# Optimization experiments

Hardware: AMD Instinct MI355X
Metric: run time of the kernel (lower is better)

Reference implementation:

```python
import jax, jax.numpy as jnp
import numpy as np

DIM = 1024
DIM_HEAD = 64
HEADS = 16
BATCH = 2
SEQ = 2048
SCALE = DIM_HEAD ** -0.5


def setup_inputs() -> dict:
    key = jax.random.key(0)
    ks = jax.random.split(key, 5)
    tokens = jax.random.normal(ks[0], (BATCH, SEQ, DIM), dtype=jnp.float32)
    wq = jax.random.normal(ks[1], (HEADS, DIM, DIM_HEAD), dtype=jnp.float32)
    wk = jax.random.normal(ks[2], (HEADS, DIM, DIM_HEAD), dtype=jnp.float32)
    wv = jax.random.normal(ks[3], (HEADS, DIM, DIM_HEAD), dtype=jnp.float32)
    wo = jax.random.normal(ks[4], (HEADS, DIM_HEAD, DIM), dtype=jnp.float32)
    return {"tokens": tokens, "wq": wq, "wk": wk, "wv": wv, "wo": wo}


def reference(tokens, wq, wk, wv, wo):
    # q, k, v: [b, h, n, dh]
    q = jnp.einsum('bnd,hde->bhne', tokens, wq) * SCALE
    k = jnp.einsum('bnd,hde->bhne', tokens, wk)
    v = jnp.einsum('bnd,hde->bhne', tokens, wv)
    sim = jnp.einsum('bhie,bhje->bhij', q, k)          # [b, h, n, n]
    attn = jax.nn.softmax(sim, axis=-1)
    aggregated = jnp.einsum('bhij,bhje->bhie', attn, v)  # [b, h, n, dh]
    retrieved = jnp.einsum('bhne,hed->bnd', aggregated, wo)  # sum over heads
    return retrieved
```

## Files before the change

kernel.cpp:

```cpp
#include <hip/hip_runtime.h>
#include <hip/hip_fp16.h>
#include <stdint.h>

#define BB 2
#define HH 16
#define SS 2048
#define DD 1024
#define DHH 64
#define QSCALE 0.18033688011112042f

typedef _Float16 half8 __attribute__((ext_vector_type(8)));
typedef _Float16 half4 __attribute__((ext_vector_type(4)));
typedef __fp16 fp16x2 __attribute__((ext_vector_type(2)));
typedef float floatx4 __attribute__((ext_vector_type(4)));

__device__ __forceinline__ floatx4 mfma16(half8 a, half8 b, floatx4 c) {
  return __builtin_amdgcn_mfma_f32_16x16x32_f16(a, b, c, 0, 0, 0);
}
__device__ __forceinline__ floatx4 mfma16k16(half4 a, half4 b, floatx4 c) {
  return __builtin_amdgcn_mfma_f32_16x16x16f16(a, b, c, 0, 0, 0);
}

__device__ __forceinline__ void dma16(const _Float16* g, _Float16* l) {
  __builtin_amdgcn_global_load_lds(
      (const __attribute__((address_space(1))) uint32_t*)g,
      (__attribute__((address_space(3))) uint32_t*)l,
      16, 0, 0);
}

__global__ __launch_bounds__(256) void convert_kernel(
    const float* __restrict__ wq, const float* __restrict__ wk,
    const float* __restrict__ wv, const float* __restrict__ wo,
    _Float16* __restrict__ Wh, _Float16* __restrict__ Wl,
    _Float16* __restrict__ Wot)
{
  __shared__ float St[64][68];
  const int kt = blockIdx.x;
  const int hy = blockIdx.y;
  const int z  = blockIdx.z;
  const int t  = (int)threadIdx.x;
  const int k0 = kt * 64;

  const float* src = (z == 0) ? (wq + hy * (DD * DHH))
                   : (z == 1) ? (wk + hy * (DD * DHH))
                   : (z == 2) ? (wv + hy * (DD * DHH))
                   : wo;

  const int rr = t >> 4, cc = (t & 15) * 4;
  if (z < 3) {
    #pragma unroll
    for (int i = 0; i < 4; ++i)
      *(floatx4*)&St[rr + 16 * i][cc] =
          *(const floatx4*)(src + (k0 + rr + 16 * i) * DHH + cc);
  } else {
    const int d0 = hy * 64;
    #pragma unroll
    for (int i = 0; i < 4; ++i)
      *(floatx4*)&St[rr + 16 * i][cc] =
          *(const floatx4*)(src + (k0 + rr + 16 * i) * 1024 + d0 + cc);
  }
  __syncthreads();

  const int e = t >> 2, kc = (t & 3) * 16;
  if (z < 3) {
    const int n = z * 1024 + hy * 64 + e;
    half8 hi0, hi1, lo0, lo1;
    #pragma unroll
    for (int u = 0; u < 16; ++u) {
      float x = St[kc + u][e];
      _Float16 hh = (_Float16)x;
      _Float16 ll = (_Float16)(x - (float)hh);
      if (u < 8) { hi0[u] = hh; lo0[u] = ll; }
      else       { hi1[u - 8] = hh; lo1[u - 8] = ll; }
    }
    *(half8*)(Wh + n * 1024 + k0 + kc)     = hi0;
    *(half8*)(Wh + n * 1024 + k0 + kc + 8) = hi1;
    *(half8*)(Wl + n * 1024 + k0 + kc)     = lo0;
    *(half8*)(Wl + n * 1024 + k0 + kc + 8) = lo1;
  } else {
    const int d0 = hy * 64;
    half8 hi0, hi1;
    #pragma unroll
    for (int u = 0; u < 16; ++u) {
      _Float16 hh = (_Float16)St[kc + u][e];
      if (u < 8) hi0[u] = hh; else hi1[u - 8] = hh;
    }
    *(half8*)(Wot + (d0 + e) * 1024 + k0 + kc)     = hi0;
    *(half8*)(Wot + (d0 + e) * 1024 + k0 + kc + 8) = hi1;
  }
}

__global__ __launch_bounds__(256) void tokens_split_kernel(
    const float* __restrict__ tokens,
    _Float16* __restrict__ th, _Float16* __restrict__ tl)
{
  const int i = ((int)blockIdx.x * 256 + (int)threadIdx.x) * 8;
  floatx4 x0 = *(const floatx4*)(tokens + i);
  floatx4 x1 = *(const floatx4*)(tokens + i + 4);
  half8 h, l;
  #pragma unroll
  for (int j = 0; j < 8; ++j) {
    float x = (j < 4) ? x0[j] : x1[j - 4];
    _Float16 hh = (_Float16)x;
    h[j] = hh;
    l[j] = (_Float16)(x - (float)hh);
  }
  *(half8*)(th + i) = h;
  *(half8*)(tl + i) = l;
}

__global__ __launch_bounds__(256) void qkv_gemm_kernel(
    const _Float16* __restrict__ th, const _Float16* __restrict__ tl,
    const _Float16* __restrict__ Wh, const _Float16* __restrict__ Wl,
    _Float16* __restrict__ qh, _Float16* __restrict__ ql,
    _Float16* __restrict__ kh, _Float16* __restrict__ kl,
    _Float16* __restrict__ vt)
{
  __shared__ alignas(16) _Float16 sbuf[2][4][128 * 32];

  const int n0 = blockIdx.x * 128;
  const int m0 = blockIdx.y * 128;
  const int zb = n0 >> 10;
  const bool is_v = (zb == 2);
  const int t = (int)threadIdx.x;
  const int lane = t & 63, wid = t >> 6;
  const int l16 = lane & 15, q4 = lane >> 4;
  const int mw = (wid & 1) * 64, nw = (wid >> 1) * 64;

  const int g  = (lane & 7) ^ ((lane >> 3) & 7);
  const int grow  = (lane >> 3) * 2 + (g >> 2);
  const int gcol8 = (g & 3) * 8;
  const int laneoff = (l16 >> 1) * 128 + (((((l16 & 1) << 2) | q4) ^ (l16 >> 1)) * 16);

  const _Float16* src;
  int arr;
  if (wid == 0)      { src = th + m0 * 1024; arr = 0; }
  else if (wid == 1) { src = Wh + n0 * 1024; arr = 1; }
  else if (wid == 2) { src = Wl + n0 * 1024; arr = 2; }
  else               { src = tl + m0 * 1024; arr = 3; }
  const bool stage_active = !(is_v && wid == 3);
  const _Float16* gsrc = src + grow * 1024 + gcol8;

  const floatx4 z4 = {0.0f, 0.0f, 0.0f, 0.0f};
  floatx4 acc[4][4];
  #pragma unroll
  for (int mi = 0; mi < 4; ++mi)
    #pragma unroll
    for (int ni = 0; ni < 4; ++ni) acc[mi][ni] = z4;

  auto stage = [&](int buf, int kt2) {
    if (stage_active) {
      const _Float16* gp = gsrc + kt2 * 32;
      _Float16* dst = &sbuf[buf][arr][0];
      #pragma unroll
      for (int j = 0; j < 8; ++j)
        dma16(gp + j * 16 * 1024, dst + j * 16 * 32);
    }
  };

  auto compute = [&](int buf) {
    const char* sAh = (const char*)&sbuf[buf][0][0];
    const char* sBh = (const char*)&sbuf[buf][1][0];
    const char* sBl = (const char*)&sbuf[buf][2][0];
    const char* sAl = (const char*)&sbuf[buf][3][0];
    half8 a_h[4];
    #pragma unroll
    for (int mi = 0; mi < 4; ++mi)
      a_h[mi] = *(const half8*)(sAh + (mw + mi * 16) * 64 + laneoff);
    if (!is_v) {
      half8 a_l[4];
      #pragma unroll
      for (int mi = 0; mi < 4; ++mi)
        a_l[mi] = *(const half8*)(sAl + (mw + mi * 16) * 64 + laneoff);
      #pragma unroll
      for (int ni = 0; ni < 4; ++ni) {
        const half8 b_h = *(const half8*)(sBh + (nw + ni * 16) * 64 + laneoff);
        const half8 b_l = *(const half8*)(sBl + (nw + ni * 16) * 64 + laneoff);
        #pragma unroll
        for (int mi = 0; mi < 4; ++mi) {
          acc[mi][ni] = mfma16(a_h[mi], b_h, acc[mi][ni]);
          acc[mi][ni] = mfma16(a_h[mi], b_l, acc[mi][ni]);
          acc[mi][ni] = mfma16(a_l[mi], b_h, acc[mi][ni]);
        }
      }
    } else {
      #pragma unroll
      for (int ni = 0; ni < 4; ++ni) {
        const half8 b_h = *(const half8*)(sBh + (nw + ni * 16) * 64 + laneoff);
        const half8 b_l = *(const half8*)(sBl + (nw + ni * 16) * 64 + laneoff);
        #pragma unroll
        for (int mi = 0; mi < 4; ++mi) {
          acc[mi][ni] = mfma16(a_h[mi], b_h, acc[mi][ni]);
          acc[mi][ni] = mfma16(a_h[mi], b_l, acc[mi][ni]);
        }
      }
    }
  };

  stage(0, 0);
  __syncthreads();

  #pragma unroll 1
  for (int kt = 0; kt < 32; kt += 2) {
    if (kt + 1 < 32) stage(1, kt + 1);
    compute(0);
    __syncthreads();
    if (kt + 2 < 32) stage(0, kt + 2);
    compute(1);
    __syncthreads();
  }

  #pragma unroll
  for (int ni = 0; ni < 4; ++ni) {
    const int ncol = n0 + nw + ni * 16;
    const int h = (ncol >> 6) & 15;
    const int e = (ncol & 63) + l16;
    #pragma unroll
    for (int mi = 0; mi < 4; ++mi) {
      #pragma unroll
      for (int r = 0; r < 4; ++r) {
        const int grow2 = m0 + mw + mi * 16 + q4 * 4 + r;
        const int b = grow2 >> 11, s = grow2 & 2047;
        const float v = acc[mi][ni][r];
        const int qkidx = ((b * HH + h) * SS + s) * DHH + e;
        if (zb == 0) {
          const float vs = v * QSCALE;
          const _Float16 hh = (_Float16)vs;
          qh[qkidx] = hh;
          ql[qkidx] = (_Float16)(vs - (float)hh);
        } else if (zb == 1) {
          const _Float16 hh = (_Float16)v;
          kh[qkidx] = hh;
          kl[qkidx] = (_Float16)(v - (float)hh);
        } else {
          vt[((b * HH + h) * DHH + e) * SS + s] = (_Float16)v;
        }
      }
    }
  }
}

__global__ __launch_bounds__(512) void attn_kernel(
    const _Float16* __restrict__ qh, const _Float16* __restrict__ ql,
    const _Float16* __restrict__ kh, const _Float16* __restrict__ kl,
    const _Float16* __restrict__ vt, _Float16* __restrict__ agg)
{
  __shared__ _Float16 Kh[2][64][72], Kl[2][64][72], Vs[2][64][72];

  const int qt = blockIdx.x;
  const int h  = blockIdx.y;
  const int b  = blockIdx.z;
  const int bh = b * HH + h;
  const int t = (int)threadIdx.x;
  const int lane = t & 63, wid = t >> 6;
  const int l16 = lane & 15, q4 = lane >> 4;

  const int sr = t >> 3, sc = (t & 7) * 8;

  half8 qfh[2], qfl[2];
  {
    const int s = qt * 128 + wid * 16 + l16;
    const int base = (bh * SS + s) * DHH + q4 * 8;
    qfh[0] = *(const half8*)(qh + base);
    qfh[1] = *(const half8*)(qh + base + 32);
    qfl[0] = *(const half8*)(ql + base);
    qfl[1] = *(const half8*)(ql + base + 32);
  }

  const floatx4 z4 = {0.0f, 0.0f, 0.0f, 0.0f};
  floatx4 o[4];
  #pragma unroll
  for (int i = 0; i < 4; ++i) o[i] = z4;
  float m_r = -1e30f;
  float l_lane = 0.0f;

  half8 pK, pL, pV;
  {
    const int gk = (bh * SS + sr) * DHH + sc;
    pK = *(const half8*)(kh + gk);
    pL = *(const half8*)(kl + gk);
    pV = *(const half8*)(vt + (bh * DHH + sr) * SS + sc);
  }

  auto body = [&](int buf, int kt) {
    *(half8*)&Kh[buf][sr][sc] = pK;
    *(half8*)&Kl[buf][sr][sc] = pL;
    *(half8*)&Vs[buf][sr][sc] = pV;
    __syncthreads();

    if (kt < 31) {
      const int k1 = (kt + 1) * 64;
      const int gk = (bh * SS + k1 + sr) * DHH + sc;
      pK = *(const half8*)(kh + gk);
      pL = *(const half8*)(kl + gk);
      pV = *(const half8*)(vt + (bh * DHH + sr) * SS + k1 + sc);
    }

    floatx4 sv[4];
    __builtin_amdgcn_s_setprio(1);
    #pragma unroll
    for (int sub = 0; sub < 4; ++sub) {
      const half8 ah0 = *(const half8*)&Kh[buf][sub * 16 + l16][q4 * 8];
      const half8 ah1 = *(const half8*)&Kh[buf][sub * 16 + l16][q4 * 8 + 32];
      const half8 al0 = *(const half8*)&Kl[buf][sub * 16 + l16][q4 * 8];
      const half8 al1 = *(const half8*)&Kl[buf][sub * 16 + l16][q4 * 8 + 32];
      floatx4 s4 = z4;
      s4 = mfma16(ah0, qfh[0], s4);
      s4 = mfma16(ah1, qfh[1], s4);
      s4 = mfma16(al0, qfh[0], s4);
      s4 = mfma16(al1, qfh[1], s4);
      s4 = mfma16(ah0, qfl[0], s4);
      s4 = mfma16(ah1, qfl[1], s4);
      sv[sub] = s4;
    }
    __builtin_amdgcn_s_setprio(0);

    float m0 = fmaxf(fmaxf(sv[0][0], sv[0][1]), fmaxf(sv[0][2], sv[0][3]));
    float m1 = fmaxf(fmaxf(sv[1][0], sv[1][1]), fmaxf(sv[1][2], sv[1][3]));
    float m2 = fmaxf(fmaxf(sv[2][0], sv[2][1]), fmaxf(sv[2][2], sv[2][3]));
    float m3 = fmaxf(fmaxf(sv[3][0], sv[3][1]), fmaxf(sv[3][2], sv[3][3]));
    const float mx = fmaxf(fmaxf(m0, m1), fmaxf(m2, m3));

    if (__any(mx > m_r + 8.0f)) {
      float mc = fmaxf(mx, __shfl_xor(mx, 16));
      mc = fmaxf(mc, __shfl_xor(mc, 32));
      const float mnew = fmaxf(m_r, mc);
      const float alpha = exp2f(m_r - mnew);
      m_r = mnew;
      l_lane *= alpha;
      #pragma unroll
      for (int sub = 0; sub < 4; ++sub)
        #pragma unroll
        for (int r = 0; r < 4; ++r) o[sub][r] *= alpha;
    }

    half4 p4[4];
    #pragma unroll
    for (int c = 0; c < 4; ++c) {
      const float p0 = exp2f(sv[c][0] - m_r);
      const float p1 = exp2f(sv[c][1] - m_r);
      const float p2 = exp2f(sv[c][2] - m_r);
      const float p3 = exp2f(sv[c][3] - m_r);
      l_lane += (p0 + p1) + (p2 + p3);
      const fp16x2 a01 = __builtin_amdgcn_cvt_pkrtz(p0, p1);
      const fp16x2 a23 = __builtin_amdgcn_cvt_pkrtz(p2, p3);
      half4 pv;
      pv[0] = (_Float16)a01[0]; pv[1] = (_Float16)a01[1];
      pv[2] = (_Float16)a23[0]; pv[3] = (_Float16)a23[1];
      p4[c] = pv;
    }

    __builtin_amdgcn_s_setprio(1);
    #pragma unroll
    for (int c = 0; c < 4; ++c) {
      #pragma unroll
      for (int sub = 0; sub < 4; ++sub) {
        const half4 va =
            *(const half4*)&Vs[buf][sub * 16 + l16][c * 16 + q4 * 4];
        o[sub] = mfma16k16(va, p4[c], o[sub]);
      }
    }
    __builtin_amdgcn_s_setprio(0);
  };

  #pragma unroll 1
  for (int kt = 0; kt < 32; kt += 2) {
    body(0, kt);
    body(1, kt + 1);
  }

  float lsum = l_lane;
  lsum += __shfl_xor(lsum, 16);
  lsum += __shfl_xor(lsum, 32);
  const float inv = 1.0f / lsum;
  const int s = qt * 128 + wid * 16 + l16;
  #pragma unroll
  for (int sub = 0; sub < 4; ++sub) {
    half4 ov;
    #pragma unroll
    for (int r = 0; r < 4; ++r) ov[r] = (_Float16)(o[sub][r] * inv);
    *(half4*)(agg + (b * SS + s) * (HH * DHH) + h * DHH + sub * 16 + q4 * 4) = ov;
  }
}

__global__ __launch_bounds__(256) void out_gemm_kernel(
    const _Float16* __restrict__ agg, const _Float16* __restrict__ Wot,
    float* __restrict__ out)
{
  __shared__ alignas(16) _Float16 sbuf[2][2][128 * 32];
  const int n0 = blockIdx.x * 128;
  const int m0 = blockIdx.y * 128;
  const int t = (int)threadIdx.x;
  const int lane = t & 63, wid = t >> 6;
  const int l16 = lane & 15, q4 = lane >> 4;
  const int mw = (wid & 1) * 64, nw = (wid >> 1) * 64;

  const int g  = (lane & 7) ^ ((lane >> 3) & 7);
  const int grow  = (lane >> 3) * 2 + (g >> 2);
  const int gcol8 = (g & 3) * 8;
  const int laneoff = (l16 >> 1) * 128 + (((((l16 & 1) << 2) | q4) ^ (l16 >> 1)) * 16);

  const int arr = wid >> 1;
  const int half64 = (wid & 1) * 64;
  const _Float16* src = (arr == 0) ? (agg + m0 * 1024) : (Wot + n0 * 1024);
  const _Float16* gsrc = src + (half64 + grow) * 1024 + gcol8;

  const floatx4 z4 = {0.0f, 0.0f, 0.0f, 0.0f};
  floatx4 acc[4][4];
  #pragma unroll
  for (int mi = 0; mi < 4; ++mi)
    #pragma unroll
    for (int ni = 0; ni < 4; ++ni) acc[mi][ni] = z4;

  auto stage = [&](int buf, int kt2) {
    const _Float16* gp = gsrc + kt2 * 32;
    _Float16* dst = &sbuf[buf][arr][half64 * 32];
    #pragma unroll
    for (int j = 0; j < 4; ++j)
      dma16(gp + j * 16 * 1024, dst + j * 16 * 32);
  };

  auto compute = [&](int buf) {
    const char* sA = (const char*)&sbuf[buf][0][0];
    const char* sB = (const char*)&sbuf[buf][1][0];
    half8 a_f[4];
    #pragma unroll
    for (int mi = 0; mi < 4; ++mi)
      a_f[mi] = *(const half8*)(sA + (mw + mi * 16) * 64 + laneoff);
    #pragma unroll
    for (int ni = 0; ni < 4; ++ni) {
      const half8 b_f = *(const half8*)(sB + (nw + ni * 16) * 64 + laneoff);
      #pragma unroll
      for (int mi = 0; mi < 4; ++mi)
        acc[mi][ni] = mfma16(a_f[mi], b_f, acc[mi][ni]);
    }
  };

  stage(0, 0);
  __syncthreads();

  #pragma unroll 1
  for (int kt = 0; kt < 32; kt += 2) {
    if (kt + 1 < 32) stage(1, kt + 1);
    compute(0);
    __syncthreads();
    if (kt + 2 < 32) stage(0, kt + 2);
    compute(1);
    __syncthreads();
  }

  #pragma unroll
  for (int ni = 0; ni < 4; ++ni)
    #pragma unroll
    for (int mi = 0; mi < 4; ++mi)
      #pragma unroll
      for (int r = 0; r < 4; ++r)
        out[(m0 + mw + mi * 16 + q4 * 4 + r) * 1024 + n0 + nw + ni * 16 + l16] =
            acc[mi][ni][r];
}

extern "C" void kernel_launch(void* const* d_in, const int* in_sizes, int n_in,
                              void* d_out, int out_size, void* d_ws, size_t ws_size,
                              hipStream_t stream)
{
  const float* tokens = (const float*)d_in[0];
  const float* wq = (const float*)d_in[1];
  const float* wk = (const float*)d_in[2];
  const float* wv = (const float*)d_in[3];
  const float* wo = (const float*)d_in[4];
  float* out = (float*)d_out;

  char* ws = (char*)d_ws;
  _Float16* qh  = (_Float16*)(ws);
  _Float16* ql  = (_Float16*)(ws + 8388608);
  _Float16* kh  = (_Float16*)(ws + 16777216);
  _Float16* kl  = (_Float16*)(ws + 25165824);
  _Float16* vt  = (_Float16*)(ws + 33554432);
  _Float16* Wh  = (_Float16*)(ws + 41943040);
  _Float16* Wl  = (_Float16*)(ws + 48234496);
  _Float16* Wot = (_Float16*)(ws + 54525952);
  _Float16* th  = (_Float16*)(ws + 56623104);
  _Float16* tl  = (_Float16*)(ws + 65011712);
  _Float16* agg = (_Float16*)(ws + 56623104);

  convert_kernel<<<dim3(16, 16, 4), 256, 0, stream>>>(wq, wk, wv, wo, Wh, Wl, Wot);
  tokens_split_kernel<<<2048, 256, 0, stream>>>(tokens, th, tl);
  qkv_gemm_kernel<<<dim3(24, 32), 256, 0, stream>>>(th, tl, Wh, Wl, qh, ql, kh, kl, vt);
  attn_kernel<<<dim3(16, 16, 2), 512, 0, stream>>>(qh, ql, kh, kl, vt, agg);
  out_gemm_kernel<<<dim3(8, 32), 256, 0, stream>>>(agg, Wot, out);
}
```

Measured before the change: 284.0 us.

## Permute V layout for wide LDS reads, XOR-swizzle V tile, restructure double-buffer sync

The projection kernel now writes V transposed with the sequence index permuted inside each 64-block, so the attention kernel can fetch the four k16 A-fragments for one sub-tile with two 16-byte LDS reads instead of four 8-byte reads. The V shared tile drops its padding and uses an XOR swizzle to avoid bank conflicts. The double-buffer pipeline is also reorganised: the next tile is stored to the other buffer mid-iteration, a prefetch is issued two tiles ahead, and there is one barrier at the end of each iteration. The aim is to cut LDS instruction count and bank conflicts and to hide global load latency better, at the cost of a more intricate index mapping that must match between the two kernels.

```diff
diff --git a/kernel.cpp b/kernel.cpp
--- a/kernel.cpp
+++ b/kernel.cpp
@@ -233,7 +233,9 @@
           kh[qkidx] = hh;
           kl[qkidx] = (_Float16)(v - (float)hh);
         } else {
-          vt[((b * HH + h) * DHH + e) * SS + s] = (_Float16)v;
+          const int sl = s & 63;
+          const int sp = (s & ~63) | ((sl & 48) >> 2) | ((sl & 12) << 2) | (sl & 3);
+          vt[((b * HH + h) * DHH + e) * SS + sp] = (_Float16)v;
         }
       }
     }
@@ -245,7 +247,8 @@
     const _Float16* __restrict__ kh, const _Float16* __restrict__ kl,
     const _Float16* __restrict__ vt, _Float16* __restrict__ agg)
 {
-  __shared__ _Float16 Kh[2][64][72], Kl[2][64][72], Vs[2][64][72];
+  __shared__ _Float16 Kh[2][64][72], Kl[2][64][72];
+  __shared__ _Float16 Vs[2][64][64];
 
   const int qt = blockIdx.x;
   const int h  = blockIdx.y;
@@ -256,6 +259,10 @@
   const int l16 = lane & 15, q4 = lane >> 4;
 
   const int sr = t >> 3, sc = (t & 7) * 8;
+  const int vsw = ((t & 7) ^ (sr & 7)) * 8;
+
+  const int vch0 = ((2 * q4 + 0) ^ (l16 & 7)) * 8;
+  const int vch1 = ((2 * q4 + 1) ^ (l16 & 7)) * 8;
 
   half8 qfh[2], qfl[2];
   {
@@ -281,21 +288,18 @@
     pL = *(const half8*)(kl + gk);
     pV = *(const half8*)(vt + (bh * DHH + sr) * SS + sc);
   }
+  *(half8*)&Kh[0][sr][sc] = pK;
+  *(half8*)&Kl[0][sr][sc] = pL;
+  *(half8*)&Vs[0][sr][vsw] = pV;
+  __syncthreads();
+  {
+    const int gk = (bh * SS + 64 + sr) * DHH + sc;
+    pK = *(const half8*)(kh + gk);
+    pL = *(const half8*)(kl + gk);
+    pV = *(const half8*)(vt + (bh * DHH + sr) * SS + 64 + sc);
+  }
 
   auto body = [&](int buf, int kt) {
-    *(half8*)&Kh[buf][sr][sc] = pK;
-    *(half8*)&Kl[buf][sr][sc] = pL;
-    *(half8*)&Vs[buf][sr][sc] = pV;
-    __syncthreads();
-
-    if (kt < 31) {
-      const int k1 = (kt + 1) * 64;
-      const int gk = (bh * SS + k1 + sr) * DHH + sc;
-      pK = *(const half8*)(kh + gk);
-      pL = *(const half8*)(kl + gk);
-      pV = *(const half8*)(vt + (bh * DHH + sr) * SS + k1 + sc);
-    }
-
     floatx4 sv[4];
     __builtin_amdgcn_s_setprio(1);
     #pragma unroll
@@ -350,17 +354,37 @@
       p4[c] = pv;
     }
 
+    if (kt < 31) {
+      *(half8*)&Kh[buf ^ 1][sr][sc] = pK;
+      *(half8*)&Kl[buf ^ 1][sr][sc] = pL;
+      *(half8*)&Vs[buf ^ 1][sr][vsw] = pV;
+    }
+
     __builtin_amdgcn_s_setprio(1);
     #pragma unroll
-    for (int c = 0; c < 4; ++c) {
-      #pragma unroll
-      for (int sub = 0; sub < 4; ++sub) {
-        const half4 va =
-            *(const half4*)&Vs[buf][sub * 16 + l16][c * 16 + q4 * 4];
-        o[sub] = mfma16k16(va, p4[c], o[sub]);
-      }
+    for (int sub = 0; sub < 4; ++sub) {
+      const half8 v01 = *(const half8*)&Vs[buf][sub * 16 + l16][vch0];
+      const half8 v23 = *(const half8*)&Vs[buf][sub * 16 + l16][vch1];
+      const half4 va0 = {v01[0], v01[1], v01[2], v01[3]};
+      const half4 va1 = {v01[4], v01[5], v01[6], v01[7]};
+      const half4 va2 = {v23[0], v23[1], v23[2], v23[3]};
+      const half4 va3 = {v23[4], v23[5], v23[6], v23[7]};
+      o[sub] = mfma16k16(va0, p4[0], o[sub]);
+      o[sub] = mfma16k16(va1, p4[1], o[sub]);
+      o[sub] = mfma16k16(va2, p4[2], o[sub]);
+      o[sub] = mfma16k16(va3, p4[3], o[sub]);
     }
     __builtin_amdgcn_s_setprio(0);
+
+    __syncthreads();
+
+    if (kt < 30) {
+      const int k2 = (kt + 2) * 64;
+      const int gk = (bh * SS + k2 + sr) * DHH + sc;
+      pK = *(const half8*)(kh + gk);
+      pL = *(const half8*)(kl + gk);
+      pV = *(const half8*)(vt + (bh * DHH + sr) * SS + k2 + sc);
+    }
   };
 
   #pragma unroll 1
```

After: 279.0 us. No clear change (-1.7%).
